# Performance work log

Hardware: AMD Instinct MI355X
Metric: run time of the kernel (lower is better)

The kernel has to match this reference:

```python
import jax, jax.numpy as jnp
import numpy as np

S = 16384          # vision tokens (one image, 128x128 patches)
HID = 1280         # vision_hidden_size
H = 16             # num heads
D = HID // H       # head_dim = 80
L = 8              # vision_depth
FF = 3456          # vision_intermediate_size
WIN = 64           # tokens per attention window
UNIT = 4           # spatial_merge_size ** 2
OUT = 2048         # vision_out_hidden_size
PV = 3 * 2 * 16 * 16  # patch volume = 1536


def setup_inputs() -> dict:
    keys = iter(jax.random.split(jax.random.key(0), 32))
    def nrm(shape, fan_in):
        return jax.random.normal(next(keys), shape, jnp.float32) * (fan_in ** -0.5)
    ang = jax.random.uniform(next(keys), (S, D // 2), jnp.float32, 0.0, 2.0 * float(np.pi))
    ang = jnp.concatenate([ang, ang], axis=-1)  # rotate_half-compatible duplicated layout
    return {
        "x": jax.random.normal(next(keys), (S, PV), jnp.float32),
        "cos": jnp.cos(ang), "sin": jnp.sin(ang),
        "cu_seqlens": jnp.arange(S // WIN + 1, dtype=jnp.int32) * WIN,
        "pe_w": nrm((PV, HID), PV), "pe_b": jnp.zeros((HID,), jnp.float32),
        "ln1_w": jnp.ones((L, HID), jnp.float32), "ln1_b": jnp.zeros((L, HID), jnp.float32),
        "qkv_w": nrm((L, HID, 3 * HID), HID), "qkv_b": jnp.zeros((L, 3 * HID), jnp.float32),
        "proj_w": nrm((L, HID, HID), HID), "proj_b": jnp.zeros((L, HID), jnp.float32),
        "ln2_w": jnp.ones((L, HID), jnp.float32), "ln2_b": jnp.zeros((L, HID), jnp.float32),
        "fc1_w": nrm((L, HID, FF), HID), "fc1_b": jnp.zeros((L, FF), jnp.float32),
        "fc2_w": nrm((L, FF, HID), FF), "fc2_b": jnp.zeros((L, HID), jnp.float32),
        "m_ln_w": jnp.ones((HID,), jnp.float32), "m_ln_b": jnp.zeros((HID,), jnp.float32),
        "m_fc1_w": nrm((UNIT * HID, UNIT * HID), UNIT * HID), "m_fc1_b": jnp.zeros((UNIT * HID,), jnp.float32),
        "m_fc2_w": nrm((UNIT * HID, OUT), UNIT * HID), "m_fc2_b": jnp.zeros((OUT,), jnp.float32),
    }


def _ln(t, w, b, eps=1e-6):
    m = jnp.mean(t, axis=-1, keepdims=True)
    v = jnp.mean((t - m) ** 2, axis=-1, keepdims=True)
    return (t - m) * jax.lax.rsqrt(v + eps) * w + b


def _forward(cu_seqlens, x, cos, sin, pe_w, pe_b, ln1_w, ln1_b, qkv_w, qkv_b,
             proj_w, proj_b, ln2_w, ln2_b, fc1_w, fc1_b, fc2_w, fc2_b,
             m_ln_w, m_ln_b, m_fc1_w, m_fc1_b, m_fc2_w, m_fc2_b):
    NW = cu_seqlens.shape[0] - 1  # uniform windows (static)
    W = S // NW
    scale = D ** -0.5
    cosr = cos[:, None, :]  # [S,1,D]
    sinr = sin[:, None, :]

    def rope(t):  # t: [S,H,D]
        t1, t2 = jnp.split(t, 2, axis=-1)
        return t * cosr + jnp.concatenate((-t2, t1), axis=-1) * sinr

    h = x @ pe_w + pe_b  # patch embed: [S, HID]

    def block(h, p):
        l1w, l1b, qw, qb, pw, pb, l2w, l2b, f1w, f1b, f2w, f2b = p
        xn = _ln(h, l1w, l1b)
        q, k, v = jnp.split(xn @ qw + qb, 3, axis=-1)
        q = rope(q.reshape(S, H, D))
        k = rope(k.reshape(S, H, D))
        v = v.reshape(S, H, D)
        # block-diagonal (windowed) attention, fp32 scores as in source
        qw_ = q.reshape(NW, W, H, D)
        kw_ = k.reshape(NW, W, H, D)
        vw_ = v.reshape(NW, W, H, D)
        scores = jnp.einsum('wqhd,wkhd->whqk', qw_, kw_) * scale
        attn = jnp.einsum('whqk,wkhd->wqhd', jax.nn.softmax(scores, axis=-1), vw_)
        h = h + (attn.reshape(S, HID) @ pw + pb)
        xn2 = _ln(h, l2w, l2b)
        h = h + (jax.nn.gelu(xn2 @ f1w + f1b, approximate=True) @ f2w + f2b)
        return h, None

    h, _ = jax.lax.scan(block, h, (ln1_w, ln1_b, qkv_w, qkv_b, proj_w, proj_b,
                                   ln2_w, ln2_b, fc1_w, fc1_b, fc2_w, fc2_b))
    # patch merger (pre-shuffle norm)
    hm = _ln(h, m_ln_w, m_ln_b).reshape(-1, UNIT * HID)  # [S/4, 5120]
    return jax.nn.gelu(hm @ m_fc1_w + m_fc1_b, approximate=True) @ m_fc2_w + m_fc2_b


def reference(x, cos, sin, cu_seqlens, pe_w, pe_b, ln1_w, ln1_b, qkv_w, qkv_b,
              proj_w, proj_b, ln2_w, ln2_b, fc1_w, fc1_b, fc2_w, fc2_b,
              m_ln_w, m_ln_b, m_fc1_w, m_fc1_b, m_fc2_w, m_fc2_b):
    return _forward(cu_seqlens, x, cos, sin, pe_w, pe_b, ln1_w, ln1_b, qkv_w, qkv_b,
                    proj_w, proj_b, ln2_w, ln2_b, fc1_w, fc1_b, fc2_w, fc2_b,
                    m_ln_w, m_ln_b, m_fc1_w, m_fc1_b, m_fc2_w, m_fc2_b)
```

## Files before the change

kernel.cpp:

```cpp
#include <hip/hip_runtime.h>

typedef unsigned short ushortT;
typedef __attribute__((ext_vector_type(8))) short short8;
typedef __attribute__((ext_vector_type(8))) unsigned short ushort8;
typedef __attribute__((ext_vector_type(4))) unsigned short ushort4v;
typedef __attribute__((ext_vector_type(4))) float f32x4;

#define DEVINL __device__ __forceinline__

DEVINL ushortT f2bf(float f) {
    unsigned u = __builtin_bit_cast(unsigned, f);
    u += 0x7FFFu + ((u >> 16) & 1u);
    return (ushortT)(u >> 16);
}
DEVINL float bf2f(ushortT h) {
    unsigned u = ((unsigned)h) << 16;
    return __builtin_bit_cast(float, u);
}
DEVINL float gelu_tanh(float x) {
    float x3 = x * x * x;
    return 0.5f * x * (1.0f + tanhf(0.7978845608028654f * (x + 0.044715f * x3)));
}

#define GLOAD_LDS16(g, l)                                                     \
    __builtin_amdgcn_global_load_lds(                                         \
        (const __attribute__((address_space(1))) void*)(g),                   \
        (__attribute__((address_space(3))) void*)(l), 16, 0, 0)

#define WAITV(n) asm volatile("s_waitcnt vmcnt(" #n ")" ::: "memory")
#define MEMFENCE() asm volatile("" ::: "memory")
#define BAR() __builtin_amdgcn_s_barrier()
#define BARF() MEMFENCE(); BAR(); MEMFENCE()

__global__ __launch_bounds__(256) void cast_bf16_4(const float* __restrict__ in,
                                                   ushortT* __restrict__ out, long n4) {
    long i = (long)blockIdx.x * 256 + threadIdx.x;
    if (i < n4) {
        const float* p = in + i * 4;
        ushort4v o;
        o[0] = f2bf(p[0]); o[1] = f2bf(p[1]); o[2] = f2bf(p[2]); o[3] = f2bf(p[3]);
        ((ushort4v*)out)[i] = o;
    }
}

__global__ __launch_bounds__(256) void transpose_cast(const float* __restrict__ in,
                                                      ushortT* __restrict__ out,
                                                      int K, int N, int Npad) {
    __shared__ float tile[32][33];
    long zi = (long)blockIdx.z * K * N;
    long zo = (long)blockIdx.z * Npad * K;
    const float* ip = in + zi;
    ushortT* op = out + zo;
    int t = threadIdx.x, bx = blockIdx.x, by = blockIdx.y;
#pragma unroll
    for (int i = 0; i < 4; i++) {
        int idx = i * 256 + t, r = idx >> 5, c = idx & 31;
        int col = bx * 32 + c;
        tile[r][c] = (col < N) ? ip[(long)(by * 32 + r) * N + col] : 0.0f;
    }
    __syncthreads();
#pragma unroll
    for (int i = 0; i < 4; i++) {
        int idx = i * 256 + t, r = idx >> 5, c = idx & 31;
        op[(long)(bx * 32 + r) * K + by * 32 + c] = f2bf(tile[c][r]);
    }
}

__global__ __launch_bounds__(256) void pad_bias(const float* __restrict__ in,
                                                float* __restrict__ out,
                                                int n_in, int n_out, int total) {
    int i = blockIdx.x * 256 + threadIdx.x;
    if (i < total) {
        int l = i / n_out, c = i % n_out;
        out[i] = (c < n_in) ? in[l * n_in + c] : 0.0f;
    }
}

__global__ __launch_bounds__(256) void ln_bf16(const ushortT* __restrict__ in,
                                               const float* __restrict__ w,
                                               const float* __restrict__ b,
                                               ushortT* __restrict__ out) {
    const int row = blockIdx.x;
    const ushortT* x = in + (long)row * 1280;
    __shared__ float red[4];
    const int t = threadIdx.x;
    float v[8];
    float s = 0.f;
    if (t < 160) {
        ushort8 u = *(const ushort8*)(x + t * 8);
#pragma unroll
        for (int i = 0; i < 8; i++) { v[i] = bf2f(u[i]); s += v[i]; }
    } else {
#pragma unroll
        for (int i = 0; i < 8; i++) v[i] = 0.f;
    }
#pragma unroll
    for (int o = 32; o > 0; o >>= 1) s += __shfl_xor(s, o);
    int wave = t >> 6;
    if ((t & 63) == 0) red[wave] = s;
    __syncthreads();
    float mean = (red[0] + red[1] + red[2] + red[3]) * (1.0f / 1280.0f);
    float q = 0.f;
    if (t < 160) {
#pragma unroll
        for (int i = 0; i < 8; i++) { float d = v[i] - mean; q += d * d; }
    }
#pragma unroll
    for (int o = 32; o > 0; o >>= 1) q += __shfl_xor(q, o);
    __syncthreads();
    if ((t & 63) == 0) red[wave] = q;
    __syncthreads();
    float var = (red[0] + red[1] + red[2] + red[3]) * (1.0f / 1280.0f);
    float rs = rsqrtf(var + 1e-6f);
    if (t < 160) {
        ushort8 o8;
#pragma unroll
        for (int i = 0; i < 8; i++) {
            int c = t * 8 + i;
            o8[i] = f2bf((v[i] - mean) * rs * w[c] + b[c]);
        }
        *(ushort8*)(out + (long)row * 1280 + t * 8) = o8;
    }
}


#define GSTAGE(mat, ls, base, ld, k0, buf)                                    \
    _Pragma("unroll") for (int j = 0; j < 2; j++) {                           \
        int c = j * 256 + t; int sr = c >> 2, sl = c & 3;                     \
        GLOAD_LDS16(mat + (base + sr) * ld + (k0) + ((sl ^ ((sr >> 1) & 3)) * 8), \
                    &ls[buf][c * 8]);                                         \
    }
#define GREAD(buf)                                                            \
    _Pragma("unroll") for (int m = 0; m < 4; m++) {                           \
        int r = wr * 64 + m * 16 + lr;                                        \
        aF[m] = *(const short8*)&lsA[buf][r * 32 + ((lg ^ ((r >> 1) & 3)) * 8)]; \
    }                                                                         \
    _Pragma("unroll") for (int n = 0; n < 4; n++) {                           \
        int r = wc * 64 + n * 16 + lr;                                        \
        bF[n] = *(const short8*)&lsB[buf][r * 32 + ((lg ^ ((r >> 1) & 3)) * 8)]; \
    }
#define GMFMA()                                                               \
    __builtin_amdgcn_s_setprio(1);                                            \
    _Pragma("unroll") for (int m = 0; m < 4; m++)                             \
    _Pragma("unroll") for (int n = 0; n < 4; n++)                             \
        acc[m][n] = __builtin_amdgcn_mfma_f32_16x16x32_bf16(                  \
            aF[m], bF[n], acc[m][n], 0, 0, 0);                                \
    __builtin_amdgcn_s_setprio(0);

template <bool OBF, bool RESB, bool GEL>
__global__ __launch_bounds__(256, 2)
void gemm_db(const ushortT* __restrict__ A, const ushortT* __restrict__ Bt,
             const float* __restrict__ bias, const ushortT* __restrict__ resb,
             void* __restrict__ out, int M, int N, int K, int lda, int ldb) {
    __shared__ ushortT lsA[2][4096];
    __shared__ ushortT lsB[2][4096];
    const int t = threadIdx.x;
    const int lane = t & 63, lr = lane & 15, lg = lane >> 4;
    const int wave = t >> 6;
    const int wr = wave >> 1, wc = wave & 1;

    const int nwg = gridDim.x, orig = blockIdx.x;
    const int q = nwg >> 3, r8 = nwg & 7;
    const int xcd = orig & 7, loc = orig >> 3;
    const int wg = (xcd < r8 ? xcd * (q + 1) : r8 * (q + 1) + (xcd - r8) * q) + loc;
    const int gx = N >> 7;
    const size_t brow = (size_t)(wg / gx) * 128;
    const size_t bcol = (size_t)(wg % gx) * 128;

    f32x4 acc[4][4];
#pragma unroll
    for (int m = 0; m < 4; m++)
#pragma unroll
        for (int n = 0; n < 4; n++) acc[m][n] = f32x4{0.f, 0.f, 0.f, 0.f};

    GSTAGE(A, lsA, brow, lda, 0, 0);
    GSTAGE(Bt, lsB, bcol, ldb, 0, 0);
    WAITV(0); BARF();

    short8 aF[4], bF[4];
    const int NT = K >> 5;
    int cur = 0;
    for (int tt = 0; tt < NT; ++tt) {
        MEMFENCE();
        GREAD(cur);
        if (tt + 1 < NT) {
            const int k1 = (tt + 1) << 5;
            GSTAGE(A, lsA, brow, lda, k1, cur ^ 1);
            GSTAGE(Bt, lsB, bcol, ldb, k1, cur ^ 1);
        }
        GMFMA();
        if (tt + 1 < NT) {
            WAITV(0);
            BARF();
        }
        cur ^= 1;
    }

#pragma unroll
    for (int m = 0; m < 4; m++) {
#pragma unroll
        for (int n = 0; n < 4; n++) {
#pragma unroll
            for (int rr = 0; rr < 4; rr++) {
                size_t row = brow + wr * 64 + m * 16 + lg * 4 + rr;
                size_t col = bcol + wc * 64 + n * 16 + lr;
                float v = acc[m][n][rr] + bias[col];
                if (RESB) v += bf2f(resb[row * N + col]);
                if (GEL) v = gelu_tanh(v);
                if (OBF) ((ushortT*)out)[row * N + col] = f2bf(v);
                else     ((float*)out)[row * N + col] = v;
            }
        }
    }
}

__global__ __launch_bounds__(256) void attn_win(const ushortT* __restrict__ qkv,
                                                const float* __restrict__ cosb,
                                                const float* __restrict__ sinb,
                                                ushortT* __restrict__ out) {
    const int w = blockIdx.x, h = blockIdx.y;
    __shared__ ushortT qs[64 * 96];
    __shared__ ushortT ks[64 * 96];
    __shared__ ushortT vt[80 * 80];
    __shared__ float   sc[64 * 65];
    __shared__ ushortT pb[64 * 80];
    const int t = threadIdx.x, wave = t >> 6, lane = t & 63, lr = lane & 15, lg = lane >> 4;
    const ushortT* bq = qkv + (long)w * 64 * 3840 + h * 80;

    for (int c = t; c < 640; c += 256) {
        int r = c / 10, cb = c % 10;
        const ushortT* qp = bq + (long)r * 3840;
        ushort8 qa = *(const ushort8*)(qp + cb * 8);
        ushort8 ka = *(const ushort8*)(qp + 1280 + cb * 8);
        int pcb = (cb < 5) ? cb + 5 : cb - 5;
        ushort8 qpr = *(const ushort8*)(qp + pcb * 8);
        ushort8 kpr = *(const ushort8*)(qp + 1280 + pcb * 8);
        long srow = (long)w * 64 + r;
        const float* cp = cosb + srow * 80 + cb * 8;
        const float* sp = sinb + srow * 80 + cb * 8;
        float sgn = (cb < 5) ? -1.f : 1.f;
        ushort8 qo, ko;
#pragma unroll
        for (int j = 0; j < 8; j++) {
            float c_ = cp[j], s_ = sp[j] * sgn;
            qo[j] = f2bf(bf2f(qa[j]) * c_ + bf2f(qpr[j]) * s_);
            ko[j] = f2bf(bf2f(ka[j]) * c_ + bf2f(kpr[j]) * s_);
        }
        *(ushort8*)&qs[r * 96 + cb * 8] = qo;
        *(ushort8*)&ks[r * 96 + cb * 8] = ko;
        ushort8 vv = *(const ushort8*)(qp + 2560 + cb * 8);
#pragma unroll
        for (int j = 0; j < 8; j++) vt[(cb * 8 + j) * 80 + r] = vv[j];
    }
    for (int idx = t; idx < 1024; idx += 256) {
        int r = idx >> 4, c2 = 80 + (idx & 15);
        qs[r * 96 + c2] = 0;
        ks[r * 96 + c2] = 0;
    }
    __syncthreads();

    f32x4 sa[4];
#pragma unroll
    for (int n = 0; n < 4; n++) sa[n] = f32x4{0.f, 0.f, 0.f, 0.f};
#pragma unroll
    for (int kk = 0; kk < 3; kk++) {
        short8 aq = *(const short8*)&qs[(wave * 16 + lr) * 96 + kk * 32 + lg * 8];
#pragma unroll
        for (int n = 0; n < 4; n++) {
            short8 bk = *(const short8*)&ks[(n * 16 + lr) * 96 + kk * 32 + lg * 8];
            sa[n] = __builtin_amdgcn_mfma_f32_16x16x32_bf16(aq, bk, sa[n], 0, 0, 0);
        }
    }
    const float scale = 0.11180339887498949f;
#pragma unroll
    for (int n = 0; n < 4; n++)
#pragma unroll
        for (int r = 0; r < 4; r++)
            sc[(wave * 16 + lg * 4 + r) * 65 + n * 16 + lr] = sa[n][r] * scale;
    __syncthreads();

    {
        int row = t >> 2, q4 = t & 3;
        float pv[16];
        float mx = -1e30f;
#pragma unroll
        for (int j = 0; j < 16; j++) { pv[j] = sc[row * 65 + q4 * 16 + j]; mx = fmaxf(mx, pv[j]); }
        mx = fmaxf(mx, __shfl_xor(mx, 1));
        mx = fmaxf(mx, __shfl_xor(mx, 2));
        float sum = 0.f;
#pragma unroll
        for (int j = 0; j < 16; j++) { pv[j] = __expf(pv[j] - mx); sum += pv[j]; }
        sum += __shfl_xor(sum, 1);
        sum += __shfl_xor(sum, 2);
        float inv = 1.0f / sum;
#pragma unroll
        for (int j = 0; j < 16; j++) pb[row * 80 + q4 * 16 + j] = f2bf(pv[j] * inv);
    }
    __syncthreads();

    f32x4 pa[5];
#pragma unroll
    for (int n = 0; n < 5; n++) pa[n] = f32x4{0.f, 0.f, 0.f, 0.f};
#pragma unroll
    for (int kk = 0; kk < 2; kk++) {
        short8 ap = *(const short8*)&pb[(wave * 16 + lr) * 80 + kk * 32 + lg * 8];
#pragma unroll
        for (int n = 0; n < 5; n++) {
            short8 bv = *(const short8*)&vt[(n * 16 + lr) * 80 + kk * 32 + lg * 8];
            pa[n] = __builtin_amdgcn_mfma_f32_16x16x32_bf16(ap, bv, pa[n], 0, 0, 0);
        }
    }
    ushortT* ob = out + (long)w * 64 * 1280 + h * 80;
#pragma unroll
    for (int n = 0; n < 5; n++)
#pragma unroll
        for (int r = 0; r < 4; r++)
            ob[(long)(wave * 16 + lg * 4 + r) * 1280 + n * 16 + lr] = f2bf(pa[n][r]);
}

extern "C" void kernel_launch(void* const* d_in, const int* in_sizes, int n_in,
                              void* d_out, int out_size, void* d_ws, size_t ws_size,
                              hipStream_t stream) {
    const float* x      = (const float*)d_in[0];
    const float* cosb   = (const float*)d_in[1];
    const float* sinb   = (const float*)d_in[2];
    const float* pe_w   = (const float*)d_in[4];
    const float* pe_b   = (const float*)d_in[5];
    const float* ln1_w  = (const float*)d_in[6];
    const float* ln1_b  = (const float*)d_in[7];
    const float* qkv_w  = (const float*)d_in[8];
    const float* qkv_b  = (const float*)d_in[9];
    const float* proj_w = (const float*)d_in[10];
    const float* proj_b = (const float*)d_in[11];
    const float* ln2_w  = (const float*)d_in[12];
    const float* ln2_b  = (const float*)d_in[13];
    const float* fc1_w  = (const float*)d_in[14];
    const float* fc1_b  = (const float*)d_in[15];
    const float* fc2_w  = (const float*)d_in[16];
    const float* fc2_b  = (const float*)d_in[17];
    const float* mln_w  = (const float*)d_in[18];
    const float* mln_b  = (const float*)d_in[19];
    const float* mfc1_w = (const float*)d_in[20];
    const float* mfc1_b = (const float*)d_in[21];
    const float* mfc2_w = (const float*)d_in[22];
    const float* mfc2_b = (const float*)d_in[23];

    char* ws = (char*)d_ws;
    size_t off = 0;
    auto alloc = [&](size_t bytes) -> char* {
        char* p = ws + off;
        off += (bytes + 255) & ~(size_t)255;
        return p;
    };
    ushortT* pe_wT   = (ushortT*)alloc((size_t)1280 * 1536 * 2);
    ushortT* qkv_wT  = (ushortT*)alloc((size_t)8 * 3840 * 1280 * 2);
    ushortT* proj_wT = (ushortT*)alloc((size_t)8 * 1280 * 1280 * 2);
    ushortT* fc1_wT  = (ushortT*)alloc((size_t)8 * 3584 * 1280 * 2);
    ushortT* fc2_wT  = (ushortT*)alloc((size_t)8 * 1280 * 3456 * 2);
    ushortT* mfc1_wT = (ushortT*)alloc((size_t)5120 * 5120 * 2);
    ushortT* mfc2_wT = (ushortT*)alloc((size_t)2048 * 5120 * 2);
    float*   fc1_bp  = (float*)alloc((size_t)8 * 3584 * 4);
    ushortT* hbuf    = (ushortT*)alloc((size_t)16384 * 1280 * 2);
    ushortT* xn      = (ushortT*)alloc((size_t)16384 * 1280 * 2);
    ushortT* big     = (ushortT*)alloc((size_t)16384 * 3840 * 2);
    ushortT* attnb   = (ushortT*)alloc((size_t)16384 * 1280 * 2);

    ushortT* xbf  = big;
    ushortT* qkvb = big;
    ushortT* ffn1 = big;
    ushortT* t1   = attnb;

    transpose_cast<<<dim3(1280 / 32, 1536 / 32, 1), 256, 0, stream>>>(pe_w,   pe_wT,   1536, 1280, 1280);
    transpose_cast<<<dim3(3840 / 32, 1280 / 32, 8), 256, 0, stream>>>(qkv_w,  qkv_wT,  1280, 3840, 3840);
    transpose_cast<<<dim3(1280 / 32, 1280 / 32, 8), 256, 0, stream>>>(proj_w, proj_wT, 1280, 1280, 1280);
    transpose_cast<<<dim3(3584 / 32, 1280 / 32, 8), 256, 0, stream>>>(fc1_w,  fc1_wT,  1280, 3456, 3584);
    transpose_cast<<<dim3(1280 / 32, 3456 / 32, 8), 256, 0, stream>>>(fc2_w,  fc2_wT,  3456, 1280, 1280);
    transpose_cast<<<dim3(5120 / 32, 5120 / 32, 1), 256, 0, stream>>>(mfc1_w, mfc1_wT, 5120, 5120, 5120);
    transpose_cast<<<dim3(2048 / 32, 5120 / 32, 1), 256, 0, stream>>>(mfc2_w, mfc2_wT, 5120, 2048, 2048);
    pad_bias<<<(8 * 3584 + 255) / 256, 256, 0, stream>>>(fc1_b, fc1_bp, 3456, 3584, 8 * 3584);

    cast_bf16_4<<<(16384L * 1536 / 4 + 255) / 256, 256, 0, stream>>>(x, xbf, 16384L * 1536 / 4);
    gemm_db<true, false, false><<<dim3(128 * 10), 256, 0, stream>>>(
        xbf, pe_wT, pe_b, nullptr, hbuf, 16384, 1280, 1536, 1536, 1536);

    for (int l = 0; l < 8; l++) {
        ln_bf16<<<16384, 256, 0, stream>>>(hbuf, ln1_w + l * 1280, ln1_b + l * 1280, xn);
        gemm_db<true, false, false><<<dim3(128 * 30), 256, 0, stream>>>(
            xn, qkv_wT + (size_t)l * 3840 * 1280, qkv_b + l * 3840, nullptr, qkvb,
            16384, 3840, 1280, 1280, 1280);
        attn_win<<<dim3(256, 16), 256, 0, stream>>>(qkvb, cosb, sinb, attnb);
        gemm_db<true, true, false><<<dim3(128 * 10), 256, 0, stream>>>(
            attnb, proj_wT + (size_t)l * 1280 * 1280, proj_b + l * 1280, hbuf, hbuf,
            16384, 1280, 1280, 1280, 1280);
        ln_bf16<<<16384, 256, 0, stream>>>(hbuf, ln2_w + l * 1280, ln2_b + l * 1280, xn);
        gemm_db<true, false, true><<<dim3(128 * 28), 256, 0, stream>>>(
            xn, fc1_wT + (size_t)l * 3584 * 1280, fc1_bp + l * 3584, nullptr, ffn1,
            16384, 3584, 1280, 1280, 1280);
        gemm_db<true, true, false><<<dim3(128 * 10), 256, 0, stream>>>(
            ffn1, fc2_wT + (size_t)l * 1280 * 3456, fc2_b + l * 1280, hbuf, hbuf,
            16384, 1280, 3456, 3584, 3456);
    }

    ln_bf16<<<16384, 256, 0, stream>>>(hbuf, mln_w, mln_b, xn);
    gemm_db<true, false, true><<<dim3(32 * 40), 256, 0, stream>>>(
        xn, mfc1_wT, mfc1_b, nullptr, t1, 4096, 5120, 5120, 5120, 5120);
    gemm_db<false, false, false><<<dim3(32 * 16), 256, 0, stream>>>(
        t1, mfc2_wT, mfc2_b, nullptr, (float*)d_out, 4096, 2048, 5120, 5120, 5120);
}
```

Before: 7.135 ms.

## Add 256x256-tile double-buffered GEMM with XCD-aware remap for QKV, FC1, merger

Introduces a new GEMM kernel using 256x256 output tiles, 512 threads (8 waves), a 64-wide K step with XOR-swizzled LDS, and a workgroup remap that gives each XCD a contiguous range of tiles. It replaces the 128x128 gemm_db launches for the QKV, FC1 and merger FC1 projections. Larger tiles cut global and L2 traffic per FLOP, and the remap improves L2 locality on each chiplet. The cost is 128 KB of LDS per block, a large accumulator register footprint that limits occupancy, and a single barrier per K step with no finer interleaving.

Measured after the change: 7.143 ms. No clear change (+0.1%).

```diff
diff --git a/kernel.cpp b/kernel.cpp
--- a/kernel.cpp
+++ b/kernel.cpp
@@ -123,11 +123,10 @@
     }
 }
 
-
 #define GSTAGE(mat, ls, base, ld, k0, buf)                                    \
     _Pragma("unroll") for (int j = 0; j < 2; j++) {                           \
         int c = j * 256 + t; int sr = c >> 2, sl = c & 3;                     \
-        GLOAD_LDS16(mat + (base + sr) * ld + (k0) + ((sl ^ ((sr >> 1) & 3)) * 8), \
+        GLOAD_LDS16(mat + (base + sr) * (size_t)ld + (k0) + ((sl ^ ((sr >> 1) & 3)) * 8), \
                     &ls[buf][c * 8]);                                         \
     }
 #define GREAD(buf)                                                            \
@@ -206,6 +205,106 @@
                 size_t col = bcol + wc * 64 + n * 16 + lr;
                 float v = acc[m][n][rr] + bias[col];
                 if (RESB) v += bf2f(resb[row * N + col]);
+                if (GEL) v = gelu_tanh(v);
+                if (OBF) ((ushortT*)out)[row * N + col] = f2bf(v);
+                else     ((float*)out)[row * N + col] = v;
+            }
+        }
+    }
+}
+
+template <int BM, int BN, int WN, bool OBF, bool GEL>
+__global__ __launch_bounds__(128 * WN, 2)
+void gemm2ph(const ushortT* __restrict__ A, const ushortT* __restrict__ Bt,
+             const float* __restrict__ bias,
+             void* __restrict__ out, int M, int N, int K, int lda, int ldb) {
+    constexpr int THREADS = 128 * WN;
+    constexpr int MR = BM / 32;
+    constexpr int NR = BN / (WN * 16);
+    constexpr int AOPS = (BM * 8) / THREADS;
+    constexpr int BOPS = (BN * 8) / THREADS;
+    __shared__ ushortT lsA[2][BM * 64];
+    __shared__ ushortT lsB[2][BN * 64];
+
+    const int t = threadIdx.x;
+    const int lane = t & 63, lr = lane & 15, lg = lane >> 4;
+    const int wave = t >> 6;
+    const int wr = wave / WN, wc = wave % WN;
+
+    const int nwg = gridDim.x;
+    const int orig = blockIdx.x;
+    const int q = nwg >> 3, r8 = nwg & 7;
+    const int xcd = orig & 7, loc = orig >> 3;
+    const int wg = (xcd < r8 ? xcd * (q + 1) : r8 * (q + 1) + (xcd - r8) * q) + loc;
+    const int gx = N / BN;
+    const int bx = wg % gx, by = wg / gx;
+    const long brow = (long)by * BM;
+    const long bcol = (long)bx * BN;
+
+    auto stage = [&](int buf, int k0) {
+#pragma unroll
+        for (int j = 0; j < AOPS; j++) {
+            int idx = j * THREADS + t;
+            int row = idx >> 3, slot = idx & 7;
+            int ss = slot ^ (row & 7);
+            GLOAD_LDS16(A + (size_t)(brow + row) * lda + k0 + ss * 8,
+                        &lsA[buf][idx * 8]);
+        }
+#pragma unroll
+        for (int j = 0; j < BOPS; j++) {
+            int idx = j * THREADS + t;
+            int row = idx >> 3, slot = idx & 7;
+            int ss = slot ^ (row & 7);
+            GLOAD_LDS16(Bt + (size_t)(bcol + row) * ldb + k0 + ss * 8,
+                        &lsB[buf][idx * 8]);
+        }
+    };
+
+    f32x4 acc[MR][NR];
+#pragma unroll
+    for (int m = 0; m < MR; m++)
+#pragma unroll
+        for (int n = 0; n < NR; n++) acc[m][n] = f32x4{0.f, 0.f, 0.f, 0.f};
+
+    stage(0, 0);
+    __syncthreads();
+
+    const int NT = K >> 6;
+    for (int tt = 0; tt < NT; tt++) {
+        const int cur = tt & 1;
+        if (tt + 1 < NT) stage(cur ^ 1, (tt + 1) << 6);
+#pragma unroll
+        for (int kk = 0; kk < 2; kk++) {
+            short8 af[MR], bfg[NR];
+#pragma unroll
+            for (int m = 0; m < MR; m++) {
+                int row = wr * (BM / 2) + m * 16 + lr;
+                af[m] = *(const short8*)&lsA[cur][row * 64 + (((kk * 4 + lg) ^ (row & 7)) * 8)];
+            }
+#pragma unroll
+            for (int n = 0; n < NR; n++) {
+                int row = wc * (BN / WN) + n * 16 + lr;
+                bfg[n] = *(const short8*)&lsB[cur][row * 64 + (((kk * 4 + lg) ^ (row & 7)) * 8)];
+            }
+#pragma unroll
+            for (int m = 0; m < MR; m++)
+#pragma unroll
+                for (int n = 0; n < NR; n++)
+                    acc[m][n] = __builtin_amdgcn_mfma_f32_16x16x32_bf16(af[m], bfg[n],
+                                                                        acc[m][n], 0, 0, 0);
+        }
+        __syncthreads();
+    }
+
+#pragma unroll
+    for (int m = 0; m < MR; m++) {
+#pragma unroll
+        for (int n = 0; n < NR; n++) {
+#pragma unroll
+            for (int rr = 0; rr < 4; rr++) {
+                size_t row = brow + wr * (BM / 2) + m * 16 + lg * 4 + rr;
+                size_t col = bcol + wc * (BN / WN) + n * 16 + lr;
+                float v = acc[m][n][rr] + bias[col];
                 if (GEL) v = gelu_tanh(v);
                 if (OBF) ((ushortT*)out)[row * N + col] = f2bf(v);
                 else     ((float*)out)[row * N + col] = v;
@@ -385,16 +484,16 @@
 
     for (int l = 0; l < 8; l++) {
         ln_bf16<<<16384, 256, 0, stream>>>(hbuf, ln1_w + l * 1280, ln1_b + l * 1280, xn);
-        gemm_db<true, false, false><<<dim3(128 * 30), 256, 0, stream>>>(
-            xn, qkv_wT + (size_t)l * 3840 * 1280, qkv_b + l * 3840, nullptr, qkvb,
+        gemm2ph<256, 256, 4, true, false><<<dim3(15 * 64), 512, 0, stream>>>(
+            xn, qkv_wT + (size_t)l * 3840 * 1280, qkv_b + l * 3840, qkvb,
             16384, 3840, 1280, 1280, 1280);
         attn_win<<<dim3(256, 16), 256, 0, stream>>>(qkvb, cosb, sinb, attnb);
         gemm_db<true, true, false><<<dim3(128 * 10), 256, 0, stream>>>(
             attnb, proj_wT + (size_t)l * 1280 * 1280, proj_b + l * 1280, hbuf, hbuf,
             16384, 1280, 1280, 1280, 1280);
         ln_bf16<<<16384, 256, 0, stream>>>(hbuf, ln2_w + l * 1280, ln2_b + l * 1280, xn);
-        gemm_db<true, false, true><<<dim3(128 * 28), 256, 0, stream>>>(
-            xn, fc1_wT + (size_t)l * 3584 * 1280, fc1_bp + l * 3584, nullptr, ffn1,
+        gemm2ph<256, 256, 4, true, true><<<dim3(14 * 64), 512, 0, stream>>>(
+            xn, fc1_wT + (size_t)l * 3584 * 1280, fc1_bp + l * 3584, ffn1,
             16384, 3584, 1280, 1280, 1280);
         gemm_db<true, true, false><<<dim3(128 * 10), 256, 0, stream>>>(
             ffn1, fc2_wT + (size_t)l * 1280 * 3456, fc2_b + l * 1280, hbuf, hbuf,
@@ -402,8 +501,8 @@
     }
 
     ln_bf16<<<16384, 256, 0, stream>>>(hbuf, mln_w, mln_b, xn);
-    gemm_db<true, false, true><<<dim3(32 * 40), 256, 0, stream>>>(
-        xn, mfc1_wT, mfc1_b, nullptr, t1, 4096, 5120, 5120, 5120, 5120);
+    gemm2ph<256, 256, 4, true, true><<<dim3(20 * 16), 512, 0, stream>>>(
+        xn, mfc1_wT, mfc1_b, t1, 4096, 5120, 5120, 5120, 5120);
     gemm_db<false, false, false><<<dim3(32 * 16), 256, 0, stream>>>(
         t1, mfc2_wT, mfc2_b, nullptr, (float*)d_out, 4096, 2048, 5120, 5120, 5120);
 }
```
